# Kernel optimization log

Hardware: AMD Instinct MI355X
Metric: run time of the kernel (lower is better)

The kernel has to match this reference:

```python
import jax, jax.numpy as jnp
import numpy as np

EPS = 1e-8


def setup_inputs() -> dict:
    key = jax.random.key(0)
    k1, k2, k3, k4 = jax.random.split(key, 4)
    B, N, M, C = 512, 512, 128, 1024
    addr = M + 6  # read head: k(M) + beta(1) + g(1) + s(3) + gamma(1)
    controller_out = jax.random.normal(k1, (B, C), dtype=jnp.float32)
    prev_w = jax.random.uniform(k2, (B, N), dtype=jnp.float32)
    prev_w = prev_w / prev_w.sum(axis=1, keepdims=True)  # valid weighting
    memory_state = jax.random.normal(k3, (B, N, M), dtype=jnp.float32)
    W_fc = jax.random.normal(k4, (C, addr), dtype=jnp.float32) * 0.02
    b_fc = jnp.zeros((addr,), dtype=jnp.float32)
    return {"controller_out": controller_out, "prev_w": prev_w,
            "memory_state": memory_state, "W_fc": W_fc, "b_fc": b_fc}


def reference(controller_out, prev_w, memory_state, W_fc, b_fc):
    M = memory_state.shape[2]
    out = controller_out @ W_fc + b_fc  # [B, M+6]
    k = out[:, :M]                                   # key
    beta = jax.nn.softplus(out[:, M:M + 1])          # key strength
    g = jax.nn.sigmoid(out[:, M + 1:M + 2])          # interpolation gate
    s = jax.nn.softmax(out[:, M + 2:M + 5], axis=1)  # 3-tap shift weights
    gamma = 1.0 + jax.nn.softplus(out[:, M + 5:M + 6])

    # Content addressing (Eq. 5-6): cosine similarity + sharpened softmax
    norm_k = jnp.linalg.norm(k, axis=1, keepdims=True) + EPS      # [B,1]
    norm_mem = jnp.linalg.norm(memory_state, axis=2) + EPS        # [B,N]
    sim = jnp.einsum('bnm,bm->bn', memory_state, k) / (norm_k * norm_mem)
    w_c = jax.nn.softmax(beta * sim, axis=1)

    # Interpolation (Eq. 7)
    w_g = g * w_c + (1.0 - g) * prev_w

    # Circular 3-tap shift (Eq. 8): vectorized roll instead of per-slot loop
    w_s = (s[:, 0:1] * jnp.roll(w_g, 1, axis=1)
           + s[:, 1:2] * w_g
           + s[:, 2:3] * jnp.roll(w_g, -1, axis=1))

    # Sharpening (Eq. 9)
    w_pow = w_s ** gamma
    w = w_pow / (w_pow.sum(axis=1, keepdims=True) + EPS)

    # Read vector (read head)
    read_vec = jnp.einsum('bn,bnm->bm', w, memory_state)
    return (read_vec, w)
```

## Files before the change

kernel.cpp:

```cpp
#include <hip/hip_runtime.h>
#include <math.h>

#define BB   512
#define NN   512
#define MM   128
#define CC   1024
#define ADDR 134
#define EPSF 1e-8f

__device__ __forceinline__ float softplus_f(float x) {
    return fmaxf(x, 0.0f) + log1pf(expf(-fabsf(x)));
}

__global__ __launch_bounds__(512) void k1_fc(
    const float* __restrict__ co, const float* __restrict__ W_fc,
    const float* __restrict__ b_fc, float* __restrict__ kk )
{
    __shared__ __align__(16) float s_co0[CC];
    __shared__ __align__(16) float s_co1[CC];
    __shared__ float s_part0[4 * MM];
    __shared__ float s_part1[4 * MM];
    __shared__ float s_beta[2];
    __shared__ float s_red[2][2];
    __shared__ float s_scale[2];

    const int t  = threadIdx.x;
    const int b0 = blockIdx.x;
    const int b1 = blockIdx.x + 256;

    s_co0[t]       = co[(size_t)b0 * CC + t];
    s_co0[t + 512] = co[(size_t)b0 * CC + t + 512];
    s_co1[t]       = co[(size_t)b1 * CC + t];
    s_co1[t + 512] = co[(size_t)b1 * CC + t + 512];
    __syncthreads();

    {
        const int o    = t & (MM - 1);
        const int part = t >> 7;
        const float* Wp = W_fc + o;
        float a0 = 0.f, a1 = 0.f, a2 = 0.f, a3 = 0.f;
        float d0 = 0.f, d1 = 0.f, d2 = 0.f, d3 = 0.f;
        const int cc0 = part * 256;
        for (int c = cc0; c < cc0 + 256; c += 4) {
            float w0 = Wp[(size_t)(c + 0) * ADDR];
            float w1 = Wp[(size_t)(c + 1) * ADDR];
            float w2 = Wp[(size_t)(c + 2) * ADDR];
            float w3 = Wp[(size_t)(c + 3) * ADDR];
            float4 u = *(const float4*)(s_co0 + c);
            float4 v = *(const float4*)(s_co1 + c);
            a0 = fmaf(u.x, w0, a0); a1 = fmaf(u.y, w1, a1);
            a2 = fmaf(u.z, w2, a2); a3 = fmaf(u.w, w3, a3);
            d0 = fmaf(v.x, w0, d0); d1 = fmaf(v.y, w1, d1);
            d2 = fmaf(v.z, w2, d2); d3 = fmaf(v.w, w3, d3);
        }
        s_part0[part * MM + o] = (a0 + a1) + (a2 + a3);
        s_part1[part * MM + o] = (d0 + d1) + (d2 + d3);

        const int wv = t >> 6;
        if (wv < 2) {
            const int ll = t & 63;
            const float* cosrc = wv ? s_co1 : s_co0;
            const float* We = W_fc + MM;
            float e = 0.f;
            for (int c = ll; c < CC; c += 64)
                e = fmaf(cosrc[c], We[(size_t)c * ADDR], e);
            #pragma unroll
            for (int off = 32; off >= 1; off >>= 1) e += __shfl_xor(e, off, 64);
            if (ll == 0) s_beta[wv] = e + b_fc[MM];
        }
    }
    __syncthreads();

    float k0 = 0.f, k1v = 0.f;
    if (t < MM) {
        float bias = b_fc[t];
        k0  = bias + s_part0[t] + s_part0[MM + t] + s_part0[2 * MM + t] + s_part0[3 * MM + t];
        k1v = bias + s_part1[t] + s_part1[MM + t] + s_part1[2 * MM + t] + s_part1[3 * MM + t];
        float v0 = k0 * k0, v1 = k1v * k1v;
        #pragma unroll
        for (int off = 32; off >= 1; off >>= 1) {
            v0 += __shfl_xor(v0, off, 64);
            v1 += __shfl_xor(v1, off, 64);
        }
        if ((t & 63) == 0) { s_red[0][t >> 6] = v0; s_red[1][t >> 6] = v1; }
    }
    __syncthreads();
    if (t < 2) {
        float ks = s_red[t][0] + s_red[t][1];
        s_scale[t] = softplus_f(s_beta[t]) / (sqrtf(ks) + EPSF);
    }
    __syncthreads();
    if (t < MM) {
        kk[(size_t)b0 * MM + t] = k0  * s_scale[0];
        kk[(size_t)b1 * MM + t] = k1v * s_scale[1];
    }
}

__global__ __launch_bounds__(256) void k2_sim(
    const float* __restrict__ mem, const float* __restrict__ kk,
    float* __restrict__ bsim )
{
    const int bb   = blockIdx.x;
    const int b    = bb >> 2;
    const int tile = bb & 3;
    const int t = threadIdx.x;
    const int g = t >> 5;
    const int l = t & 31;
    const float4* memb = (const float4*)(mem + (size_t)b * NN * MM) + (size_t)tile * 128 * 32;
    const float4 kv = ((const float4*)(kk + (size_t)b * MM))[l];
    float* bs = bsim + (size_t)b * NN + tile * 128;

    #pragma unroll
    for (int j = 0; j < 16; j += 4) {
        float4 a0 = memb[(size_t)(g + (j + 0) * 8) * 32 + l];
        float4 a1 = memb[(size_t)(g + (j + 1) * 8) * 32 + l];
        float4 a2 = memb[(size_t)(g + (j + 2) * 8) * 32 + l];
        float4 a3 = memb[(size_t)(g + (j + 3) * 8) * 32 + l];

        float d0 = a0.x*kv.x + a0.y*kv.y + a0.z*kv.z + a0.w*kv.w;
        float d1 = a1.x*kv.x + a1.y*kv.y + a1.z*kv.z + a1.w*kv.w;
        float d2 = a2.x*kv.x + a2.y*kv.y + a2.z*kv.z + a2.w*kv.w;
        float d3 = a3.x*kv.x + a3.y*kv.y + a3.z*kv.z + a3.w*kv.w;
        float q0 = a0.x*a0.x + a0.y*a0.y + a0.z*a0.z + a0.w*a0.w;
        float q1 = a1.x*a1.x + a1.y*a1.y + a1.z*a1.z + a1.w*a1.w;
        float q2 = a2.x*a2.x + a2.y*a2.y + a2.z*a2.z + a2.w*a2.w;
        float q3 = a3.x*a3.x + a3.y*a3.y + a3.z*a3.z + a3.w*a3.w;

        d0 += __shfl_xor(d0, 16, 64); q0 += __shfl_xor(q0, 16, 64);
        d1 += __shfl_xor(d1, 16, 64); q1 += __shfl_xor(q1, 16, 64);
        d2 += __shfl_xor(d2, 16, 64); q2 += __shfl_xor(q2, 16, 64);
        d3 += __shfl_xor(d3, 16, 64); q3 += __shfl_xor(q3, 16, 64);
        float W0 = (l & 16) ? q0 : d0;
        float W1 = (l & 16) ? q1 : d1;
        float W2 = (l & 16) ? q2 : d2;
        float W3 = (l & 16) ? q3 : d3;
        W0 += __shfl_xor(W0, 8, 64); W1 += __shfl_xor(W1, 8, 64);
        W2 += __shfl_xor(W2, 8, 64); W3 += __shfl_xor(W3, 8, 64);
        float X0 = (l & 8) ? W1 : W0;
        float X1 = (l & 8) ? W3 : W2;
        X0 += __shfl_xor(X0, 4, 64); X1 += __shfl_xor(X1, 4, 64);
        float Y = (l & 4) ? X1 : X0;
        Y += __shfl_xor(Y, 2, 64);
        Y += __shfl_xor(Y, 1, 64);
        float Q = __shfl_xor(Y, 16, 64);
        if (l < 16 && (l & 3) == 0) {
            int jj = j + ((l & 4) >> 1) + ((l & 8) >> 3);
            bs[g + jj * 8] = Y / (sqrtf(Q) + EPSF);
        }
    }
}

__global__ __launch_bounds__(1024) void k3_tail(
    const float* __restrict__ co, const float* __restrict__ prev_w,
    const float* __restrict__ mem, const float* __restrict__ W_fc,
    const float* __restrict__ b_fc,
    float* __restrict__ out_rv, float* __restrict__ out_w)
{
    __shared__ float s_wg[NN];
    __shared__ float s_w[NN];
    __shared__ __align__(16) float s_part[32 * MM];
    __shared__ float s_scr[4 * MM];
    __shared__ float s_red[16];
    __shared__ float s_ex[16][8];
    __shared__ float s_params[8];

    const int t = threadIdx.x;
    const int b = blockIdx.x;
    const int gi = t >> 5;
    const int l  = t & 31;
    const float4* memb = (const float4*)(mem + (size_t)b * NN * MM);

    float covt = co[(size_t)b * CC + t];
    const float* We = W_fc + (size_t)t * ADDR + (MM + 1);
    float ex0 = covt * We[0];
    float ex1 = covt * We[1];
    float ex2 = covt * We[2];
    float ex3 = covt * We[3];
    float ex4 = covt * We[4];

    float pw = (t < NN) ? prev_w[(size_t)b * NN + t] : 0.0f;
    const float NEG = -3.0e38f;
    float b1 = (t < NN) ? out_w[(size_t)b * NN + t] : NEG;

    float m = b1;
    #pragma unroll
    for (int off = 32; off >= 1; off >>= 1) {
        m = fmaxf(m, __shfl_xor(m, off, 64));
        ex0 += __shfl_xor(ex0, off, 64);
        ex1 += __shfl_xor(ex1, off, 64);
        ex2 += __shfl_xor(ex2, off, 64);
        ex3 += __shfl_xor(ex3, off, 64);
        ex4 += __shfl_xor(ex4, off, 64);
    }
    if ((t & 63) == 0) {
        const int w = t >> 6;
        s_red[w] = m;
        s_ex[w][0] = ex0; s_ex[w][1] = ex1; s_ex[w][2] = ex2;
        s_ex[w][3] = ex3; s_ex[w][4] = ex4;
    }
    __syncthreads();

    if (t == 0) {
        float t0 = 0.f, t1 = 0.f, t2 = 0.f, t3 = 0.f, t4 = 0.f;
        #pragma unroll
        for (int w = 0; w < 16; ++w) {
            t0 += s_ex[w][0]; t1 += s_ex[w][1]; t2 += s_ex[w][2];
            t3 += s_ex[w][3]; t4 += s_ex[w][4];
        }
        t0 += b_fc[MM + 1]; t1 += b_fc[MM + 2]; t2 += b_fc[MM + 3];
        t3 += b_fc[MM + 4]; t4 += b_fc[MM + 5];
        float g = 1.0f / (1.0f + expf(-t0));
        float mx = fmaxf(t1, fmaxf(t2, t3));
        float x0 = expf(t1 - mx), x1 = expf(t2 - mx), x2 = expf(t3 - mx);
        float inv = 1.0f / (x0 + x1 + x2);
        s_params[0] = g;
        s_params[1] = x0 * inv; s_params[2] = x1 * inv; s_params[3] = x2 * inv;
        s_params[4] = 1.0f + softplus_f(t4);
    }
    float M8 = s_red[0];
    #pragma unroll
    for (int i = 1; i < 8; ++i) M8 = fmaxf(M8, s_red[i]);
    __syncthreads();

    float e1 = (t < NN) ? expf(b1 - M8) : 0.0f;
    float ls = e1;
    #pragma unroll
    for (int off = 32; off >= 1; off >>= 1) ls += __shfl_xor(ls, off, 64);
    if ((t & 63) == 0) s_red[t >> 6] = ls;
    __syncthreads();
    float S = s_red[0];
    #pragma unroll
    for (int i = 1; i < 8; ++i) S += s_red[i];
    __syncthreads();

    const float invS = 1.0f / S;
    const float g = s_params[0];
    float wg1 = fmaf(g, e1 * invS, (1.0f - g) * pw);
    if (t < NN) s_wg[t] = wg1;
    __syncthreads();

    const float sh0 = s_params[1], sh1 = s_params[2], sh2 = s_params[3];
    const float gamma = s_params[4];
    float wp1 = 0.0f;
    if (t < NN) {
        float ws1 = sh0 * s_wg[(t + NN - 1) & (NN - 1)]
                  + sh1 * wg1
                  + sh2 * s_wg[(t + 1) & (NN - 1)];
        wp1 = powf(ws1, gamma);
        s_w[t] = wp1;
    }
    __syncthreads();

    float4 acc = make_float4(0.f, 0.f, 0.f, 0.f);
    for (int j = 0; j < 16; j += 4) {
        float4 a0 = memb[(size_t)(gi + (j + 0) * 32) * 32 + l];
        float4 a1 = memb[(size_t)(gi + (j + 1) * 32) * 32 + l];
        float4 a2 = memb[(size_t)(gi + (j + 2) * 32) * 32 + l];
        float4 a3 = memb[(size_t)(gi + (j + 3) * 32) * 32 + l];
        float w0 = s_w[gi + (j + 0) * 32];
        float w1 = s_w[gi + (j + 1) * 32];
        float w2 = s_w[gi + (j + 2) * 32];
        float w3 = s_w[gi + (j + 3) * 32];
        acc.x = fmaf(w0, a0.x, acc.x); acc.y = fmaf(w0, a0.y, acc.y);
        acc.z = fmaf(w0, a0.z, acc.z); acc.w = fmaf(w0, a0.w, acc.w);
        acc.x = fmaf(w1, a1.x, acc.x); acc.y = fmaf(w1, a1.y, acc.y);
        acc.z = fmaf(w1, a1.z, acc.z); acc.w = fmaf(w1, a1.w, acc.w);
        acc.x = fmaf(w2, a2.x, acc.x); acc.y = fmaf(w2, a2.y, acc.y);
        acc.z = fmaf(w2, a2.z, acc.z); acc.w = fmaf(w2, a2.w, acc.w);
        acc.x = fmaf(w3, a3.x, acc.x); acc.y = fmaf(w3, a3.y, acc.y);
        acc.z = fmaf(w3, a3.z, acc.z); acc.w = fmaf(w3, a3.w, acc.w);
    }

    float lz = wp1;
    #pragma unroll
    for (int off = 32; off >= 1; off >>= 1) lz += __shfl_xor(lz, off, 64);
    if ((t & 63) == 0) s_red[t >> 6] = lz;

    *((float4*)&s_part[gi * MM + l * 4]) = acc;
    __syncthreads();

    float Z = s_red[0];
    #pragma unroll
    for (int i = 1; i < 8; ++i) Z += s_red[i];
    const float invZ = 1.0f / (Z + EPSF);

    if (t < NN) out_w[(size_t)b * NN + t] = wp1 * invZ;

    if (t < 512) {
        const int h = t >> 7;
        const int o = t & (MM - 1);
        float r = 0.f;
        #pragma unroll
        for (int q = 0; q < 8; ++q) r += s_part[(h * 8 + q) * MM + o];
        s_scr[h * MM + o] = r;
    }
    __syncthreads();
    if (t < MM) {
        float r = s_scr[t] + s_scr[MM + t] + s_scr[2 * MM + t] + s_scr[3 * MM + t];
        out_rv[(size_t)b * MM + t] = r * invZ;
    }
}

extern "C" void kernel_launch(void* const* d_in, const int* in_sizes, int n_in,
                              void* d_out, int out_size, void* d_ws, size_t ws_size,
                              hipStream_t stream) {
    const float* co     = (const float*)d_in[0];
    const float* prev_w = (const float*)d_in[1];
    const float* mem    = (const float*)d_in[2];
    const float* W_fc   = (const float*)d_in[3];
    const float* b_fc   = (const float*)d_in[4];
    float* out    = (float*)d_out;
    float* out_rv = out;
    float* out_w  = out + (size_t)BB * MM;

    k1_fc  <<<256,  512, 0, stream>>>(co, W_fc, b_fc, out_rv);
    k2_sim <<<2048, 256, 0, stream>>>(mem, out_rv, out_w);
    k3_tail<<<512, 1024, 0, stream>>>(co, prev_w, mem, W_fc, b_fc, out_rv, out_w);
}
```

Baseline: 256.6 us.

## Split tail kernel into softmax kernel and tiled read kernel with atomics

Separates the weighting computation from the memory read: a 512-thread kernel computes the final normalized weights and zeroes the read vector, then a new 2048-block kernel reads each batch's memory in four row tiles and accumulates partial read vectors with atomicAdd. This raises parallelism and occupancy for the bandwidth-bound read pass, which previously ran as 512 blocks of 1024 threads. It adds one extra kernel launch, global atomics, and a write/read round trip of the weights.

```diff
diff --git a/kernel.cpp b/kernel.cpp
--- a/kernel.cpp
+++ b/kernel.cpp
@@ -150,37 +150,31 @@
     }
 }
 
-__global__ __launch_bounds__(1024) void k3_tail(
+__global__ __launch_bounds__(512) void k3_soft(
     const float* __restrict__ co, const float* __restrict__ prev_w,
-    const float* __restrict__ mem, const float* __restrict__ W_fc,
-    const float* __restrict__ b_fc,
+    const float* __restrict__ W_fc, const float* __restrict__ b_fc,
     float* __restrict__ out_rv, float* __restrict__ out_w)
 {
     __shared__ float s_wg[NN];
-    __shared__ float s_w[NN];
-    __shared__ __align__(16) float s_part[32 * MM];
-    __shared__ float s_scr[4 * MM];
-    __shared__ float s_red[16];
-    __shared__ float s_ex[16][8];
+    __shared__ float s_red[8];
+    __shared__ float s_ex[8][8];
     __shared__ float s_params[8];
 
     const int t = threadIdx.x;
     const int b = blockIdx.x;
-    const int gi = t >> 5;
-    const int l  = t & 31;
-    const float4* memb = (const float4*)(mem + (size_t)b * NN * MM);
-
-    float covt = co[(size_t)b * CC + t];
-    const float* We = W_fc + (size_t)t * ADDR + (MM + 1);
-    float ex0 = covt * We[0];
-    float ex1 = covt * We[1];
-    float ex2 = covt * We[2];
-    float ex3 = covt * We[3];
-    float ex4 = covt * We[4];
-
-    float pw = (t < NN) ? prev_w[(size_t)b * NN + t] : 0.0f;
-    const float NEG = -3.0e38f;
-    float b1 = (t < NN) ? out_w[(size_t)b * NN + t] : NEG;
+
+    float cv0 = co[(size_t)b * CC + t];
+    float cv1 = co[(size_t)b * CC + t + 512];
+    const float* We0 = W_fc + (size_t)t * ADDR + (MM + 1);
+    const float* We1 = W_fc + (size_t)(t + 512) * ADDR + (MM + 1);
+    float ex0 = cv0 * We0[0] + cv1 * We1[0];
+    float ex1 = cv0 * We0[1] + cv1 * We1[1];
+    float ex2 = cv0 * We0[2] + cv1 * We1[2];
+    float ex3 = cv0 * We0[3] + cv1 * We1[3];
+    float ex4 = cv0 * We0[4] + cv1 * We1[4];
+
+    float pw = prev_w[(size_t)b * NN + t];
+    float b1 = out_w[(size_t)b * NN + t];
 
     float m = b1;
     #pragma unroll
@@ -203,7 +197,7 @@
     if (t == 0) {
         float t0 = 0.f, t1 = 0.f, t2 = 0.f, t3 = 0.f, t4 = 0.f;
         #pragma unroll
-        for (int w = 0; w < 16; ++w) {
+        for (int w = 0; w < 8; ++w) {
             t0 += s_ex[w][0]; t1 += s_ex[w][1]; t2 += s_ex[w][2];
             t3 += s_ex[w][3]; t4 += s_ex[w][4];
         }
@@ -222,7 +216,7 @@
     for (int i = 1; i < 8; ++i) M8 = fmaxf(M8, s_red[i]);
     __syncthreads();
 
-    float e1 = (t < NN) ? expf(b1 - M8) : 0.0f;
+    float e1 = expf(b1 - M8);
     float ls = e1;
     #pragma unroll
     for (int off = 32; off >= 1; off >>= 1) ls += __shfl_xor(ls, off, 64);
@@ -236,68 +230,66 @@
     const float invS = 1.0f / S;
     const float g = s_params[0];
     float wg1 = fmaf(g, e1 * invS, (1.0f - g) * pw);
-    if (t < NN) s_wg[t] = wg1;
+    s_wg[t] = wg1;
     __syncthreads();
 
     const float sh0 = s_params[1], sh1 = s_params[2], sh2 = s_params[3];
     const float gamma = s_params[4];
-    float wp1 = 0.0f;
-    if (t < NN) {
-        float ws1 = sh0 * s_wg[(t + NN - 1) & (NN - 1)]
-                  + sh1 * wg1
-                  + sh2 * s_wg[(t + 1) & (NN - 1)];
-        wp1 = powf(ws1, gamma);
-        s_w[t] = wp1;
-    }
-    __syncthreads();
-
-    float4 acc = make_float4(0.f, 0.f, 0.f, 0.f);
-    for (int j = 0; j < 16; j += 4) {
-        float4 a0 = memb[(size_t)(gi + (j + 0) * 32) * 32 + l];
-        float4 a1 = memb[(size_t)(gi + (j + 1) * 32) * 32 + l];
-        float4 a2 = memb[(size_t)(gi + (j + 2) * 32) * 32 + l];
-        float4 a3 = memb[(size_t)(gi + (j + 3) * 32) * 32 + l];
-        float w0 = s_w[gi + (j + 0) * 32];
-        float w1 = s_w[gi + (j + 1) * 32];
-        float w2 = s_w[gi + (j + 2) * 32];
-        float w3 = s_w[gi + (j + 3) * 32];
-        acc.x = fmaf(w0, a0.x, acc.x); acc.y = fmaf(w0, a0.y, acc.y);
-        acc.z = fmaf(w0, a0.z, acc.z); acc.w = fmaf(w0, a0.w, acc.w);
-        acc.x = fmaf(w1, a1.x, acc.x); acc.y = fmaf(w1, a1.y, acc.y);
-        acc.z = fmaf(w1, a1.z, acc.z); acc.w = fmaf(w1, a1.w, acc.w);
-        acc.x = fmaf(w2, a2.x, acc.x); acc.y = fmaf(w2, a2.y, acc.y);
-        acc.z = fmaf(w2, a2.z, acc.z); acc.w = fmaf(w2, a2.w, acc.w);
-        acc.x = fmaf(w3, a3.x, acc.x); acc.y = fmaf(w3, a3.y, acc.y);
-        acc.z = fmaf(w3, a3.z, acc.z); acc.w = fmaf(w3, a3.w, acc.w);
-    }
+    float ws1 = sh0 * s_wg[(t + NN - 1) & (NN - 1)]
+              + sh1 * wg1
+              + sh2 * s_wg[(t + 1) & (NN - 1)];
+    float wp1 = powf(ws1, gamma);
 
     float lz = wp1;
     #pragma unroll
     for (int off = 32; off >= 1; off >>= 1) lz += __shfl_xor(lz, off, 64);
     if ((t & 63) == 0) s_red[t >> 6] = lz;
-
-    *((float4*)&s_part[gi * MM + l * 4]) = acc;
-    __syncthreads();
-
+    __syncthreads();
     float Z = s_red[0];
     #pragma unroll
     for (int i = 1; i < 8; ++i) Z += s_red[i];
-    const float invZ = 1.0f / (Z + EPSF);
-
-    if (t < NN) out_w[(size_t)b * NN + t] = wp1 * invZ;
-
-    if (t < 512) {
-        const int h = t >> 7;
-        const int o = t & (MM - 1);
+
+    out_w[(size_t)b * NN + t] = wp1 / (Z + EPSF);
+    if (t < MM) out_rv[(size_t)b * MM + t] = 0.0f;
+}
+
+__global__ __launch_bounds__(256) void k4_read(
+    const float* __restrict__ mem, const float* __restrict__ w,
+    float* __restrict__ out_rv)
+{
+    __shared__ float s_w[128];
+    __shared__ __align__(16) float s_part[8 * MM];
+
+    const int bb   = blockIdx.x;
+    const int b    = bb >> 2;
+    const int tile = bb & 3;
+    const int t = threadIdx.x;
+    const int g = t >> 5;
+    const int l = t & 31;
+    const float4* memb = (const float4*)(mem + (size_t)b * NN * MM) + (size_t)tile * 128 * 32;
+
+    if (t < 128) s_w[t] = w[(size_t)b * NN + tile * 128 + t];
+    __syncthreads();
+
+    float4 acc = make_float4(0.f, 0.f, 0.f, 0.f);
+    #pragma unroll
+    for (int jj = 0; jj < 16; ++jj) {
+        const int r = g + jj * 8;
+        float4 a = memb[(size_t)r * 32 + l];
+        float wv = s_w[r];
+        acc.x = fmaf(wv, a.x, acc.x);
+        acc.y = fmaf(wv, a.y, acc.y);
+        acc.z = fmaf(wv, a.z, acc.z);
+        acc.w = fmaf(wv, a.w, acc.w);
+    }
+    *((float4*)&s_part[g * MM + l * 4]) = acc;
+    __syncthreads();
+
+    if (t < MM) {
         float r = 0.f;
         #pragma unroll
-        for (int q = 0; q < 8; ++q) r += s_part[(h * 8 + q) * MM + o];
-        s_scr[h * MM + o] = r;
-    }
-    __syncthreads();
-    if (t < MM) {
-        float r = s_scr[t] + s_scr[MM + t] + s_scr[2 * MM + t] + s_scr[3 * MM + t];
-        out_rv[(size_t)b * MM + t] = r * invZ;
+        for (int q = 0; q < 8; ++q) r += s_part[q * MM + t];
+        atomicAdd(out_rv + (size_t)b * MM + t, r);
     }
 }
 
@@ -315,5 +307,6 @@
 
     k1_fc  <<<256,  512, 0, stream>>>(co, W_fc, b_fc, out_rv);
     k2_sim <<<2048, 256, 0, stream>>>(mem, out_rv, out_w);
-    k3_tail<<<512, 1024, 0, stream>>>(co, prev_w, mem, W_fc, b_fc, out_rv, out_w);
-}
+    k3_soft<<<512,  512, 0, stream>>>(co, prev_w, W_fc, b_fc, out_rv, out_w);
+    k4_read<<<2048, 256, 0, stream>>>(mem, out_w, out_rv);
+}
```

New measurement: 250.4 us. 2.4% less time.
